# Kernel optimization log

Hardware: AMD Instinct MI355X
Metric: run time of the kernel (lower is better)

The kernel has to match this reference:

```python
import jax, jax.numpy as jnp
import numpy as np

B, S, E, H = 4, 2048, 1024, 16
D = E // H  # head_dim = 64

def setup_inputs() -> dict:
    key = jax.random.key(0)
    k1, k2, k3 = jax.random.split(key, 3)
    x = jax.random.normal(k1, (B, S, E), dtype=jnp.float32)
    # nn.Linear(E, 3E, bias=False): y = x @ W^T; we store W already transposed as [E, 3E]
    w_qkv = jax.random.normal(k2, (E, 3 * E), dtype=jnp.float32) * (E ** -0.5)
    w_out = jax.random.normal(k3, (E, E), dtype=jnp.float32) * (E ** -0.5)
    b_out = jnp.zeros((E,), dtype=jnp.float32)
    return {"x": x, "w_qkv": w_qkv, "w_out": w_out, "b_out": b_out}

def reference(x, w_qkv, w_out, b_out):
    b, s, e = x.shape
    h, d = H, e // H
    # qkv projection then rearrange 'b s (qkv h d) -> qkv b h s d'
    qkv = (x @ w_qkv).reshape(b, s, 3, h, d).transpose(2, 0, 3, 1, 4)
    q, k, v = qkv[0], qkv[1], qkv[2]            # each [b, h, s, d]
    scale = jnp.asarray(d, x.dtype) ** -0.5
    att = jnp.einsum('bhxd,bhyd->bhxy', q, k) * scale   # [b, h, s, s]
    att = jax.nn.softmax(att, axis=-1)
    o = jnp.einsum('bhxy,bhyd->bhxd', att, v)           # [b, h, s, d]
    o = o.transpose(0, 2, 1, 3).reshape(b, s, e)        # 'b h s d -> b s (h d)'
    return o @ w_out + b_out
```

## Files before the change

### kernel.cpp

```cpp
#include <hip/hip_runtime.h>
#include <cstdint>
#include <cstddef>


typedef __attribute__((ext_vector_type(8))) short short8;
typedef __attribute__((ext_vector_type(4))) float float4_;
typedef unsigned int u32;
typedef unsigned short u16;

__device__ __forceinline__ u16 f2b(float f) {
  u32 u = __float_as_uint(f);
  u += 0x7FFFu + ((u >> 16) & 1u);
  return (u16)(u >> 16);
}

__device__ __forceinline__ float fexp2(float x) {
#if __has_builtin(__builtin_amdgcn_exp2f)
  return __builtin_amdgcn_exp2f(x);
#else
  return exp2f(x);
#endif
}

__device__ __forceinline__ u32 pk_trunc(float lo, float hi) {
#if __has_builtin(__builtin_amdgcn_perm)
  return __builtin_amdgcn_perm(__float_as_uint(hi), __float_as_uint(lo), 0x07060302);
#else
  return (__float_as_uint(hi) & 0xFFFF0000u) | (__float_as_uint(lo) >> 16);
#endif
}

__device__ __forceinline__ void async_cp16(const void* g, void* l) {
  __builtin_amdgcn_global_load_lds(
      (const __attribute__((address_space(1))) u32*)g,
      (__attribute__((address_space(3))) u32*)l, 16, 0, 0);
}


__global__ void cvt_x_bf16(const float* __restrict__ in, u16* __restrict__ out, int n4) {
  int i = blockIdx.x * 256 + threadIdx.x;
  if (i >= n4) return;
  float4 v = ((const float4*)in)[i];
  uint2 p;
  p.x = (u32)f2b(v.x) | ((u32)f2b(v.y) << 16);
  p.y = (u32)f2b(v.z) | ((u32)f2b(v.w) << 16);
  ((uint2*)out)[i] = p;
}

__global__ void transpose_bf16(const float* __restrict__ in, u16* __restrict__ out,
                               int R, int C) {
  __shared__ float t[32][33];
  int tx = threadIdx.x & 31, ty = threadIdx.x >> 5;
  int r0 = blockIdx.y * 32, c0 = blockIdx.x * 32;
#pragma unroll
  for (int k = 0; k < 4; k++)
    t[ty + 8 * k][tx] = in[(size_t)(r0 + ty + 8 * k) * C + c0 + tx];
  __syncthreads();
#pragma unroll
  for (int k = 0; k < 4; k++)
    out[(size_t)(c0 + ty + 8 * k) * R + r0 + tx] = f2b(t[tx][ty + 8 * k]);
}

__global__ void transpose_v(const u16* __restrict__ V, u16* __restrict__ Vt) {
  __shared__ u16 t[64][80];
  int bh = blockIdx.y, s0 = blockIdx.x * 64;
  const u16* Vh = V + (size_t)bh * 2048 * 64;
  u16* Vth = Vt + (size_t)bh * 64 * 2048;
  int tr = threadIdx.x >> 3;
  int tc = (threadIdx.x & 7) * 8;
#pragma unroll
  for (int p = 0; p < 2; p++) {
    int r = p * 32 + tr;
    *(uint4*)&t[r][tc] = *(const uint4*)(Vh + (size_t)(s0 + r) * 64 + tc);
  }
  __syncthreads();
#pragma unroll
  for (int p = 0; p < 2; p++) {
    int d = p * 32 + tr;
    u16 tmp[8];
#pragma unroll
    for (int k = 0; k < 8; k++) tmp[k] = t[tc + k][d];
    *(uint4*)(Vth + (size_t)d * 2048 + s0 + tc) = *(uint4*)tmp;
  }
}


__global__ __launch_bounds__(256) void gemm_qkv_kernel(
    const u16* __restrict__ A, const u16* __restrict__ Bt,
    u16* __restrict__ QKV) {
  const int K = 1024;
  __shared__ short8 lA[512];
  __shared__ short8 lB[512];
  int tid = threadIdx.x;
  int w = tid >> 6, l = tid & 63, lr = l & 15, lq = l >> 4;
  int m0 = blockIdx.y * 128, n0 = blockIdx.x * 128;
  int wm = w & 1, wn = w >> 1;
  float4_ acc[4][4] = {};

  const u16* gA0 = A + (size_t)(m0 + w * 32 + lr) * K + lq * 8;
  const u16* gA1 = gA0 + 16 * K;
  const u16* gB0 = Bt + (size_t)(n0 + w * 32 + lr) * K + lq * 8;
  const u16* gB1 = gB0 + 16 * K;
  short8* dA0 = &lA[(w * 2) * 64 + l];
  short8* dA1 = &lA[(w * 2 + 1) * 64 + l];
  short8* dB0 = &lB[(w * 2) * 64 + l];
  short8* dB1 = &lB[(w * 2 + 1) * 64 + l];

  for (int k0 = 0; k0 < K; k0 += 32) {
    __syncthreads();
    async_cp16(gA0 + k0, dA0);
    async_cp16(gA1 + k0, dA1);
    async_cp16(gB0 + k0, dB0);
    async_cp16(gB1 + k0, dB1);
    __syncthreads();
    short8 af[4], bf[4];
#pragma unroll
    for (int t = 0; t < 4; t++) {
      af[t] = lA[(wm * 4 + t) * 64 + l];
      bf[t] = lB[(wn * 4 + t) * 64 + l];
    }
#pragma unroll
    for (int mt = 0; mt < 4; mt++)
#pragma unroll
      for (int nt = 0; nt < 4; nt++)
        acc[mt][nt] = __builtin_amdgcn_mfma_f32_16x16x32_bf16(af[mt], bf[nt], acc[mt][nt], 0, 0, 0);
  }
  const float qsc = 0.18033688011112042f;
#pragma unroll
  for (int nt = 0; nt < 4; nt++) {
    int gn = n0 + wn * 64 + nt * 16 + lr;
    int sel = gn >> 10;
    int h = (gn >> 6) & 15;
    int d = gn & 63;
    float sc = (sel == 0) ? qsc : 1.0f;
    u16* dst = QKV + (size_t)sel * 8388608 + ((size_t)h * 2048) * 64 + d;
#pragma unroll
    for (int mt = 0; mt < 4; mt++) {
#pragma unroll
      for (int r = 0; r < 4; r++) {
        int gm = m0 + wm * 64 + mt * 16 + lq * 4 + r;
        int b = gm >> 11, s = gm & 2047;
        dst[((size_t)b * 16 * 2048 + s) * 64] = f2b(acc[mt][nt][r] * sc);
      }
    }
  }
}

__global__ __launch_bounds__(256) void gemm_out_kernel(
    const u16* __restrict__ A, const u16* __restrict__ Bt,
    const float* __restrict__ bias, float* __restrict__ out) {
  const int K = 1024;
  __shared__ short8 lA[512];
  __shared__ short8 lB[512];
  int tid = threadIdx.x;
  int w = tid >> 6, l = tid & 63, lr = l & 15, lq = l >> 4;
  int m0 = blockIdx.y * 128, n0 = blockIdx.x * 128;
  int wm = w & 1, wn = w >> 1;
  float4_ acc[4][4] = {};

  const u16* gA0 = A + (size_t)(m0 + w * 32 + lr) * K + lq * 8;
  const u16* gA1 = gA0 + 16 * K;
  const u16* gB0 = Bt + (size_t)(n0 + w * 32 + lr) * K + lq * 8;
  const u16* gB1 = gB0 + 16 * K;
  short8* dA0 = &lA[(w * 2) * 64 + l];
  short8* dA1 = &lA[(w * 2 + 1) * 64 + l];
  short8* dB0 = &lB[(w * 2) * 64 + l];
  short8* dB1 = &lB[(w * 2 + 1) * 64 + l];

  for (int k0 = 0; k0 < K; k0 += 32) {
    __syncthreads();
    async_cp16(gA0 + k0, dA0);
    async_cp16(gA1 + k0, dA1);
    async_cp16(gB0 + k0, dB0);
    async_cp16(gB1 + k0, dB1);
    __syncthreads();
    short8 af[4], bf[4];
#pragma unroll
    for (int t = 0; t < 4; t++) {
      af[t] = lA[(wm * 4 + t) * 64 + l];
      bf[t] = lB[(wn * 4 + t) * 64 + l];
    }
#pragma unroll
    for (int mt = 0; mt < 4; mt++)
#pragma unroll
      for (int nt = 0; nt < 4; nt++)
        acc[mt][nt] = __builtin_amdgcn_mfma_f32_16x16x32_bf16(af[mt], bf[nt], acc[mt][nt], 0, 0, 0);
  }
#pragma unroll
  for (int nt = 0; nt < 4; nt++) {
    int gn = n0 + wn * 64 + nt * 16 + lr;
    float bv = bias[gn];
#pragma unroll
    for (int mt = 0; mt < 4; mt++)
#pragma unroll
      for (int r = 0; r < 4; r++) {
        int gm = m0 + wm * 64 + mt * 16 + lq * 4 + r;
        out[(size_t)gm * 1024 + gn] = acc[mt][nt][r] + bv;
      }
  }
}


__global__ __launch_bounds__(256) void attn_kernel(
    const u16* __restrict__ Qb, const u16* __restrict__ Kb,
    const u16* __restrict__ Vt, u16* __restrict__ Ob) {
  const int S = 2048, D = 64;
  __shared__ short8 lK[512];
  __shared__ short8 lV[512];
  __shared__ __align__(16) u32 pb[4][16][20];
  int tid = threadIdx.x;
  int w = tid >> 6, l = tid & 63, lr = l & 15, lq = l >> 4;
  int gid = blockIdx.x;
  int xcd = gid & 7, j = gid >> 3;
  int bh = xcd * 8 + (j & 7);
  int qblk = j >> 3;
  int q0 = qblk * 128 + w * 32;
  const u16* Qh = Qb + (size_t)bh * S * D;
  const u16* Kh = Kb + (size_t)bh * S * D;
  const u16* Vh = Vt + (size_t)bh * D * S;

  short8 qf[2][2];
#pragma unroll
  for (int qg = 0; qg < 2; qg++) {
    qf[qg][0] = *(const short8*)(Qh + (q0 + qg * 16 + lr) * D + lq * 8);
    qf[qg][1] = *(const short8*)(Qh + (q0 + qg * 16 + lr) * D + 32 + lq * 8);
  }

  float ls[2][4] = {};
  float4_ o[2][4] = {};

  const u16* kg = Kh + (size_t)(((w >> 1) << 5) + 2 * lr + (w & 1)) * D + lq * 8;
  const u16* vg = Vh + (size_t)(w * 16 + lr) * S + lq * 8;
  short8* dK0 = &lK[(w * 2 + 0) * 64 + l];
  short8* dK1 = &lK[(w * 2 + 1) * 64 + l];
  short8* dV0 = &lV[(w * 2 + 0) * 64 + l];
  short8* dV1 = &lV[(w * 2 + 1) * 64 + l];

  for (int kv0 = 0; kv0 < S; kv0 += 64) {
    __syncthreads();
    async_cp16(kg + (size_t)kv0 * D, dK0);
    async_cp16(kg + (size_t)kv0 * D + 32, dK1);
    async_cp16(vg + kv0, dV0);
    async_cp16(vg + kv0 + 32, dV1);
    __syncthreads();

#pragma unroll
    for (int sub = 0; sub < 2; sub++) {
      short8 ke0 = lK[((sub * 2 + 0) * 2 + 0) * 64 + l];
      short8 ke1 = lK[((sub * 2 + 0) * 2 + 1) * 64 + l];
      short8 ko0 = lK[((sub * 2 + 1) * 2 + 0) * 64 + l];
      short8 ko1 = lK[((sub * 2 + 1) * 2 + 1) * 64 + l];
#pragma unroll
      for (int qg = 0; qg < 2; qg++) {
        float4_ z = {0.f, 0.f, 0.f, 0.f};
        float4_ s0 = __builtin_amdgcn_mfma_f32_16x16x32_bf16(qf[qg][0], ke0, z, 0, 0, 0);
        s0 = __builtin_amdgcn_mfma_f32_16x16x32_bf16(qf[qg][1], ke1, s0, 0, 0, 0);
        float4_ s1 = __builtin_amdgcn_mfma_f32_16x16x32_bf16(qf[qg][0], ko0, z, 0, 0, 0);
        s1 = __builtin_amdgcn_mfma_f32_16x16x32_bf16(qf[qg][1], ko1, s1, 0, 0, 0);
#pragma unroll
        for (int r = 0; r < 4; r++) {
          float p0 = fexp2(s0[r]);
          float p1 = fexp2(s1[r]);
          u32 pk = pk_trunc(p0, p1);
          ls[qg][r] += __uint_as_float(pk << 16) + __uint_as_float(pk & 0xFFFF0000u);
          pb[w][lq * 4 + r][lr] = pk;
        }
        short8 pa = *(const short8*)&pb[w][lr][lq * 4];
#pragma unroll
        for (int dt = 0; dt < 4; dt++)
          o[qg][dt] = __builtin_amdgcn_mfma_f32_16x16x32_bf16(
              pa, lV[(dt * 2 + sub) * 64 + l], o[qg][dt], 0, 0, 0);
      }
    }
  }

  int b = bh >> 4, h = bh & 15;
#pragma unroll
  for (int qg = 0; qg < 2; qg++) {
    float inv[4];
#pragma unroll
    for (int r = 0; r < 4; r++) {
      float s = ls[qg][r];
#pragma unroll
      for (int off = 1; off < 16; off <<= 1) s += __shfl_xor(s, off, 64);
      inv[r] = 1.0f / s;
    }
#pragma unroll
    for (int dt = 0; dt < 4; dt++)
#pragma unroll
      for (int r = 0; r < 4; r++) {
        int s_ = q0 + qg * 16 + lq * 4 + r;
        Ob[((size_t)(b * 2048 + s_)) * 1024 + h * 64 + dt * 16 + lr] =
            f2b(o[qg][dt][r] * inv[r]);
      }
  }
}


extern "C" void kernel_launch(void* const* d_in, const int* in_sizes, int n_in,
                              void* d_out, int out_size, void* d_ws, size_t ws_size,
                              hipStream_t stream) {
  const float* x     = (const float*)d_in[0];
  const float* w_qkv = (const float*)d_in[1];
  const float* w_out = (const float*)d_in[2];
  const float* b_out = (const float*)d_in[3];
  float* out = (float*)d_out;

  char* ws = (char*)d_ws;
  u16* Xb  = (u16*)(ws);
  u16* Wqt = (u16*)(ws + (16u << 20));
  u16* Wot = (u16*)(ws + (22u << 20));
  u16* QKV = (u16*)(ws + (24u << 20));
  u16* Qb  = QKV;
  u16* Kb  = QKV + 8388608;
  u16* Vb  = QKV + 16777216;
  u16* Vt  = (u16*)(ws + (72u << 20));
  u16* Ob  = Xb;

  cvt_x_bf16<<<8192, 256, 0, stream>>>(x, Xb, 2097152);
  transpose_bf16<<<dim3(96, 32), 256, 0, stream>>>(w_qkv, Wqt, 1024, 3072);
  transpose_bf16<<<dim3(32, 32), 256, 0, stream>>>(w_out, Wot, 1024, 1024);
  gemm_qkv_kernel<<<dim3(24, 64), 256, 0, stream>>>(Xb, Wqt, QKV);
  transpose_v<<<dim3(32, 64), 256, 0, stream>>>(Vb, Vt);
  attn_kernel<<<1024, 256, 0, stream>>>(Qb, Kb, Vt, Ob);
  gemm_out_kernel<<<dim3(8, 64), 256, 0, stream>>>(Ob, Wot, b_out, out);
}
```

Baseline: 348.4 us.

## Double-buffer LDS tiles and remap block indices for XCD locality

Converts the QKV GEMM, output GEMM and attention K/V loops to double-buffered shared memory, issuing the next tile's async copies before computing on the current one, which halves the barriers per tile. It also replaces the 2D grids with 1D grids whose block index is remapped so blocks on the same XCD share row tiles or attention heads, improving L2 reuse. The cost is doubled LDS per block, which may lower occupancy, and reliance on the async copy completing before the next barrier.

```diff
diff --git a/kernel.cpp b/kernel.cpp
--- a/kernel.cpp
+++ b/kernel.cpp
@@ -89,11 +89,14 @@
     const u16* __restrict__ A, const u16* __restrict__ Bt,
     u16* __restrict__ QKV) {
   const int K = 1024;
-  __shared__ short8 lA[512];
-  __shared__ short8 lB[512];
+  __shared__ short8 lA[2][512];
+  __shared__ short8 lB[2][512];
   int tid = threadIdx.x;
   int w = tid >> 6, l = tid & 63, lr = l & 15, lq = l >> 4;
-  int m0 = blockIdx.y * 128, n0 = blockIdx.x * 128;
+  int gid = blockIdx.x;
+  int xcd = gid & 7, j = gid >> 3;
+  int yloc = j & 7, xt = j >> 3;
+  int m0 = (xcd * 8 + yloc) * 128, n0 = xt * 128;
   int wm = w & 1, wn = w >> 1;
   float4_ acc[4][4] = {};
 
@@ -101,30 +104,37 @@
   const u16* gA1 = gA0 + 16 * K;
   const u16* gB0 = Bt + (size_t)(n0 + w * 32 + lr) * K + lq * 8;
   const u16* gB1 = gB0 + 16 * K;
-  short8* dA0 = &lA[(w * 2) * 64 + l];
-  short8* dA1 = &lA[(w * 2 + 1) * 64 + l];
-  short8* dB0 = &lB[(w * 2) * 64 + l];
-  short8* dB1 = &lB[(w * 2 + 1) * 64 + l];
-
-  for (int k0 = 0; k0 < K; k0 += 32) {
-    __syncthreads();
-    async_cp16(gA0 + k0, dA0);
-    async_cp16(gA1 + k0, dA1);
-    async_cp16(gB0 + k0, dB0);
-    async_cp16(gB1 + k0, dB1);
-    __syncthreads();
+
+  auto stage = [&](int buf, int k0) {
+    async_cp16(gA0 + k0, &lA[buf][(w * 2 + 0) * 64 + l]);
+    async_cp16(gA1 + k0, &lA[buf][(w * 2 + 1) * 64 + l]);
+    async_cp16(gB0 + k0, &lB[buf][(w * 2 + 0) * 64 + l]);
+    async_cp16(gB1 + k0, &lB[buf][(w * 2 + 1) * 64 + l]);
+  };
+  auto compute = [&](int buf) {
     short8 af[4], bf[4];
 #pragma unroll
     for (int t = 0; t < 4; t++) {
-      af[t] = lA[(wm * 4 + t) * 64 + l];
-      bf[t] = lB[(wn * 4 + t) * 64 + l];
+      af[t] = lA[buf][(wm * 4 + t) * 64 + l];
+      bf[t] = lB[buf][(wn * 4 + t) * 64 + l];
     }
 #pragma unroll
     for (int mt = 0; mt < 4; mt++)
 #pragma unroll
       for (int nt = 0; nt < 4; nt++)
         acc[mt][nt] = __builtin_amdgcn_mfma_f32_16x16x32_bf16(af[mt], bf[nt], acc[mt][nt], 0, 0, 0);
-  }
+  };
+
+  stage(0, 0);
+  for (int k0 = 0; k0 < K; k0 += 64) {
+    __syncthreads();
+    stage(1, k0 + 32);
+    compute(0);
+    __syncthreads();
+    if (k0 + 64 < K) stage(0, k0 + 64);
+    compute(1);
+  }
+
   const float qsc = 0.18033688011112042f;
 #pragma unroll
   for (int nt = 0; nt < 4; nt++) {
@@ -150,11 +160,14 @@
     const u16* __restrict__ A, const u16* __restrict__ Bt,
     const float* __restrict__ bias, float* __restrict__ out) {
   const int K = 1024;
-  __shared__ short8 lA[512];
-  __shared__ short8 lB[512];
+  __shared__ short8 lA[2][512];
+  __shared__ short8 lB[2][512];
   int tid = threadIdx.x;
   int w = tid >> 6, l = tid & 63, lr = l & 15, lq = l >> 4;
-  int m0 = blockIdx.y * 128, n0 = blockIdx.x * 128;
+  int gid = blockIdx.x;
+  int xcd = gid & 7, j = gid >> 3;
+  int yloc = j & 7, xt = j >> 3;
+  int m0 = (xcd * 8 + yloc) * 128, n0 = xt * 128;
   int wm = w & 1, wn = w >> 1;
   float4_ acc[4][4] = {};
 
@@ -162,30 +175,37 @@
   const u16* gA1 = gA0 + 16 * K;
   const u16* gB0 = Bt + (size_t)(n0 + w * 32 + lr) * K + lq * 8;
   const u16* gB1 = gB0 + 16 * K;
-  short8* dA0 = &lA[(w * 2) * 64 + l];
-  short8* dA1 = &lA[(w * 2 + 1) * 64 + l];
-  short8* dB0 = &lB[(w * 2) * 64 + l];
-  short8* dB1 = &lB[(w * 2 + 1) * 64 + l];
-
-  for (int k0 = 0; k0 < K; k0 += 32) {
-    __syncthreads();
-    async_cp16(gA0 + k0, dA0);
-    async_cp16(gA1 + k0, dA1);
-    async_cp16(gB0 + k0, dB0);
-    async_cp16(gB1 + k0, dB1);
-    __syncthreads();
+
+  auto stage = [&](int buf, int k0) {
+    async_cp16(gA0 + k0, &lA[buf][(w * 2 + 0) * 64 + l]);
+    async_cp16(gA1 + k0, &lA[buf][(w * 2 + 1) * 64 + l]);
+    async_cp16(gB0 + k0, &lB[buf][(w * 2 + 0) * 64 + l]);
+    async_cp16(gB1 + k0, &lB[buf][(w * 2 + 1) * 64 + l]);
+  };
+  auto compute = [&](int buf) {
     short8 af[4], bf[4];
 #pragma unroll
     for (int t = 0; t < 4; t++) {
-      af[t] = lA[(wm * 4 + t) * 64 + l];
-      bf[t] = lB[(wn * 4 + t) * 64 + l];
+      af[t] = lA[buf][(wm * 4 + t) * 64 + l];
+      bf[t] = lB[buf][(wn * 4 + t) * 64 + l];
     }
 #pragma unroll
     for (int mt = 0; mt < 4; mt++)
 #pragma unroll
       for (int nt = 0; nt < 4; nt++)
         acc[mt][nt] = __builtin_amdgcn_mfma_f32_16x16x32_bf16(af[mt], bf[nt], acc[mt][nt], 0, 0, 0);
-  }
+  };
+
+  stage(0, 0);
+  for (int k0 = 0; k0 < K; k0 += 64) {
+    __syncthreads();
+    stage(1, k0 + 32);
+    compute(0);
+    __syncthreads();
+    if (k0 + 64 < K) stage(0, k0 + 64);
+    compute(1);
+  }
+
 #pragma unroll
   for (int nt = 0; nt < 4; nt++) {
     int gn = n0 + wn * 64 + nt * 16 + lr;
@@ -205,15 +225,15 @@
     const u16* __restrict__ Qb, const u16* __restrict__ Kb,
     const u16* __restrict__ Vt, u16* __restrict__ Ob) {
   const int S = 2048, D = 64;
-  __shared__ short8 lK[512];
-  __shared__ short8 lV[512];
+  __shared__ short8 lK[2][512];
+  __shared__ short8 lV[2][512];
   __shared__ __align__(16) u32 pb[4][16][20];
   int tid = threadIdx.x;
   int w = tid >> 6, l = tid & 63, lr = l & 15, lq = l >> 4;
   int gid = blockIdx.x;
   int xcd = gid & 7, j = gid >> 3;
-  int bh = xcd * 8 + (j & 7);
-  int qblk = j >> 3;
+  int bh = xcd * 8 + (j >> 4);
+  int qblk = j & 15;
   int q0 = qblk * 128 + w * 32;
   const u16* Qh = Qb + (size_t)bh * S * D;
   const u16* Kh = Kb + (size_t)bh * S * D;
@@ -231,25 +251,21 @@
 
   const u16* kg = Kh + (size_t)(((w >> 1) << 5) + 2 * lr + (w & 1)) * D + lq * 8;
   const u16* vg = Vh + (size_t)(w * 16 + lr) * S + lq * 8;
-  short8* dK0 = &lK[(w * 2 + 0) * 64 + l];
-  short8* dK1 = &lK[(w * 2 + 1) * 64 + l];
-  short8* dV0 = &lV[(w * 2 + 0) * 64 + l];
-  short8* dV1 = &lV[(w * 2 + 1) * 64 + l];
-
-  for (int kv0 = 0; kv0 < S; kv0 += 64) {
-    __syncthreads();
-    async_cp16(kg + (size_t)kv0 * D, dK0);
-    async_cp16(kg + (size_t)kv0 * D + 32, dK1);
-    async_cp16(vg + kv0, dV0);
-    async_cp16(vg + kv0 + 32, dV1);
-    __syncthreads();
-
+
+  auto stage = [&](int buf, int kv0) {
+    async_cp16(kg + (size_t)kv0 * D, &lK[buf][(w * 2 + 0) * 64 + l]);
+    async_cp16(kg + (size_t)kv0 * D + 32, &lK[buf][(w * 2 + 1) * 64 + l]);
+    async_cp16(vg + kv0, &lV[buf][(w * 2 + 0) * 64 + l]);
+    async_cp16(vg + kv0 + 32, &lV[buf][(w * 2 + 1) * 64 + l]);
+  };
+
+  auto compute = [&](int buf) {
 #pragma unroll
     for (int sub = 0; sub < 2; sub++) {
-      short8 ke0 = lK[((sub * 2 + 0) * 2 + 0) * 64 + l];
-      short8 ke1 = lK[((sub * 2 + 0) * 2 + 1) * 64 + l];
-      short8 ko0 = lK[((sub * 2 + 1) * 2 + 0) * 64 + l];
-      short8 ko1 = lK[((sub * 2 + 1) * 2 + 1) * 64 + l];
+      short8 ke0 = lK[buf][((sub * 2 + 0) * 2 + 0) * 64 + l];
+      short8 ke1 = lK[buf][((sub * 2 + 0) * 2 + 1) * 64 + l];
+      short8 ko0 = lK[buf][((sub * 2 + 1) * 2 + 0) * 64 + l];
+      short8 ko1 = lK[buf][((sub * 2 + 1) * 2 + 1) * 64 + l];
 #pragma unroll
       for (int qg = 0; qg < 2; qg++) {
         float4_ z = {0.f, 0.f, 0.f, 0.f};
@@ -269,9 +285,19 @@
 #pragma unroll
         for (int dt = 0; dt < 4; dt++)
           o[qg][dt] = __builtin_amdgcn_mfma_f32_16x16x32_bf16(
-              pa, lV[(dt * 2 + sub) * 64 + l], o[qg][dt], 0, 0, 0);
+              pa, lV[buf][(dt * 2 + sub) * 64 + l], o[qg][dt], 0, 0, 0);
       }
     }
+  };
+
+  stage(0, 0);
+  for (int kv0 = 0; kv0 < S; kv0 += 128) {
+    __syncthreads();
+    stage(1, kv0 + 64);
+    compute(0);
+    __syncthreads();
+    if (kv0 + 128 < S) stage(0, kv0 + 128);
+    compute(1);
   }
 
   int b = bh >> 4, h = bh & 15;
@@ -320,8 +346,8 @@
   cvt_x_bf16<<<8192, 256, 0, stream>>>(x, Xb, 2097152);
   transpose_bf16<<<dim3(96, 32), 256, 0, stream>>>(w_qkv, Wqt, 1024, 3072);
   transpose_bf16<<<dim3(32, 32), 256, 0, stream>>>(w_out, Wot, 1024, 1024);
-  gemm_qkv_kernel<<<dim3(24, 64), 256, 0, stream>>>(Xb, Wqt, QKV);
+  gemm_qkv_kernel<<<1536, 256, 0, stream>>>(Xb, Wqt, QKV);
   transpose_v<<<dim3(32, 64), 256, 0, stream>>>(Vb, Vt);
   attn_kernel<<<1024, 256, 0, stream>>>(Qb, Kb, Vt, Ob);
-  gemm_out_kernel<<<dim3(8, 64), 256, 0, stream>>>(Ob, Wot, b_out, out);
-}
+  gemm_out_kernel<<<512, 256, 0, stream>>>(Ob, Wot, b_out, out);
+}
```

Measured after the change: 350.5 us. Within noise of the previous version (+0.6%).
